# Kernel tuning notes

Measured on AMD Instinct MI355X. Metric: run time of the kernel, lower is better.

The kernel has to match this reference:

```python
import jax, jax.numpy as jnp
import numpy as np

EPS = 1e-5


def _in_relu(y):
    # instance norm (no affine, biased var, eps=1e-5) + ReLU, y: [B,C,H,W]
    mu = jnp.mean(y, axis=(-2, -1), keepdims=True)
    var = jnp.mean((y - mu) ** 2, axis=(-2, -1), keepdims=True)
    return jax.nn.relu((y - mu) * jax.lax.rsqrt(var + EPS))


def _conv3(x, w, b):
    # x: [C,H,W], w: [O,I,3,3] -> [O,H,W]
    y = jax.lax.conv_general_dilated(x[None], w, (1, 1), ((1, 1), (1, 1)),
                                     dimension_numbers=('NCHW', 'OIHW', 'NCHW'))[0]
    return y + b[:, None, None]


def _mod_block(x, W, b, mod):
    # per-sample weight modulation: mod[n] * W, then conv+IN+relu; x: [B,C,H,W], mod: [B,O,I,3,3]
    y = jax.vmap(lambda xi, mi: _conv3(xi, mi * W, b))(x, mod)
    return _in_relu(y)


def _maxpool2(x):
    return jax.lax.reduce_window(x, -jnp.inf, jax.lax.max, (1, 1, 2, 2), (1, 1, 2, 2), 'VALID')


def _up2(x):
    B, C, H, W = x.shape
    # bilinear, half-pixel centers == PyTorch align_corners=False
    return jax.image.resize(x, (B, C, 2 * H, 2 * W), method='bilinear')


def _conv1x1(x, w, b):
    y = jax.lax.conv_general_dilated(x, w, (1, 1), 'VALID',
                                     dimension_numbers=('NCHW', 'OIHW', 'NCHW'))
    return y + b[None, :, None, None]


def setup_inputs() -> dict:
    key = jax.random.key(0)
    B, H, W = 8, 256, 256
    ks = iter(jax.random.split(key, 64))
    d = {}
    d['us_query_input'] = jax.random.normal(next(ks), (B, 1, H, W), jnp.float32)
    d['ksp_query_imgs'] = jax.random.normal(next(ks), (B, H, W, 2), jnp.float32)
    d['ksp_mask_query'] = jax.random.uniform(next(ks), (B, H, W), jnp.float32)
    down_io = [(1, 32), (32, 64), (64, 128), (128, 256)]
    up_io = [(512, 128), (256, 64), (128, 32), (64, 32)]
    for i, (ci, co) in enumerate(down_io):
        d[f'down_mod_{i}'] = jax.random.normal(next(ks), (B, co, ci, 3, 3), jnp.float32)
        d[f'W_d{i}'] = 0.05 * jax.random.normal(next(ks), (co, ci, 3, 3), jnp.float32)
        d[f'b_d{i}'] = 0.05 * jax.random.normal(next(ks), (co,), jnp.float32)
    d['latent_mod'] = jax.random.normal(next(ks), (B, 256, 256, 3, 3), jnp.float32)
    d['W_lat'] = 0.05 * jax.random.normal(next(ks), (256, 256, 3, 3), jnp.float32)
    d['b_lat'] = 0.05 * jax.random.normal(next(ks), (256,), jnp.float32)
    for i, (ci, co) in enumerate(up_io):
        d[f'up_mod_{i}'] = jax.random.normal(next(ks), (B, co, ci, 3, 3), jnp.float32)
        d[f'W_u{i}'] = 0.05 * jax.random.normal(next(ks), (co, ci, 3, 3), jnp.float32)
        d[f'b_u{i}'] = 0.05 * jax.random.normal(next(ks), (co,), jnp.float32)
    d['w_c1'] = 0.05 * jax.random.normal(next(ks), (16, 32, 1, 1), jnp.float32)
    d['b_c1'] = 0.05 * jax.random.normal(next(ks), (16,), jnp.float32)
    d['w_c2'] = 0.05 * jax.random.normal(next(ks), (1, 16, 1, 1), jnp.float32)
    d['b_c2'] = 0.05 * jax.random.normal(next(ks), (1,), jnp.float32)
    d['w_c3'] = 0.05 * jax.random.normal(next(ks), (1, 1, 1, 1), jnp.float32)
    d['b_c3'] = 0.05 * jax.random.normal(next(ks), (1,), jnp.float32)
    return d


def reference(us_query_input, ksp_query_imgs, ksp_mask_query,
              down_mod_0, down_mod_1, down_mod_2, down_mod_3,
              latent_mod, up_mod_0, up_mod_1, up_mod_2, up_mod_3,
              W_d0, b_d0, W_d1, b_d1, W_d2, b_d2, W_d3, b_d3,
              W_lat, b_lat,
              W_u0, b_u0, W_u1, b_u1, W_u2, b_u2, W_u3, b_u3,
              w_c1, b_c1, w_c2, b_c2, w_c3, b_c3):
    x0 = us_query_input
    out = x0
    skips = []
    downs = [(W_d0, b_d0, down_mod_0), (W_d1, b_d1, down_mod_1),
             (W_d2, b_d2, down_mod_2), (W_d3, b_d3, down_mod_3)]
    for Wc, bc, m in downs:
        out = _mod_block(out, Wc, bc, m)
        skips.append(out)
        out = _maxpool2(out)
    out = _mod_block(out, W_lat, b_lat, latent_mod)
    ups = [(W_u0, b_u0, up_mod_0), (W_u1, b_u1, up_mod_1),
           (W_u2, b_u2, up_mod_2), (W_u3, b_u3, up_mod_3)]
    for Wc, bc, m in ups:
        out = _up2(out)
        out = jnp.concatenate([out, skips.pop()], axis=1)
        out = _mod_block(out, Wc, bc, m)
    out = _conv1x1(_conv1x1(_conv1x1(out, w_c1, b_c1), w_c2, b_c2), w_c3, b_c3)
    out = out + x0
    # FFT data consistency
    pred = out[:, 0]                                  # [B,H,W]
    kpred = jnp.fft.fft2(pred, norm='ortho')
    ksp = ksp_query_imgs[..., 0] + 1j * ksp_query_imgs[..., 1]
    upd = ksp_mask_query * ksp + (1.0 - ksp_mask_query) * kpred
    img = jnp.fft.ifft2(upd, norm='ortho')
    return jnp.real(img)[:, None].astype(jnp.float32)   # [B,1,H,W]
```

## Files before the change

### kernel.cpp

```cpp
#include <hip/hip_runtime.h>


#define EPS_IN 1e-5f

typedef __attribute__((ext_vector_type(8))) short short8;
typedef __attribute__((ext_vector_type(4))) short short4_t;
typedef __attribute__((ext_vector_type(4))) float f32x4;

__device__ __forceinline__ short f2bf(float f) {
    unsigned u = __float_as_uint(f);
    unsigned r = (u + 0x7fffu + ((u >> 16) & 1u)) >> 16;
    return (short)r;
}
__device__ __forceinline__ float bf2f(short s) {
    return __uint_as_float(((unsigned)(unsigned short)s) << 16);
}

__global__ void zero_f(float* __restrict__ p, int n)
{
    int i = blockIdx.x * 256 + threadIdx.x;
    if (i < n) p[i] = 0.f;
}

__global__ void make_wm(const float* __restrict__ W, const float* __restrict__ mod,
                        short* __restrict__ wm, int Co, int Ci)
{
    int idx = blockIdx.x * 256 + threadIdx.x;
    int total = 8 * Co * Ci;
    if (idx >= total) return;
    int ci = idx % Ci;
    int rem = idx / Ci;
    int co = rem % Co;
    int b = rem / Co;
    const float* wp = W + (size_t)(co * Ci + ci) * 9;
    const float* mp = mod + ((size_t)((size_t)b * Co + co) * Ci + ci) * 9;
#pragma unroll
    for (int k = 0; k < 9; ++k)
        wm[(((size_t)(b * 9 + k) * Co + co) * Ci + ci)] = f2bf(wp[k] * mp[k]);
}

template <int VR, int NCOG>
__global__ __launch_bounds__(256) void conv3x3_cl(
    const short* __restrict__ x1, int Ci1,
    const short* __restrict__ x2,
    const short* __restrict__ wm,
    short* __restrict__ y,
    float2* __restrict__ stats,
    int Ci, int Co, int H, int W)
{
    constexpr int TH = 4 * VR, SH = TH + 2, SW = 18;
    __shared__ short s_x[SH][SW][32];
    __shared__ float s_red[4][4][NCOG][4][2];

    const int tid = threadIdx.x;
    const int lane = tid & 63, wv = tid >> 6;
    const int m = lane & 15, g = lane >> 4;
    const int tilesx = W >> 4;
    const int tx0 = (blockIdx.x % tilesx) * 16;
    const int ty0 = (blockIdx.x / tilesx) * TH;
    const int co0 = blockIdx.y * (16 * NCOG);
    const int b = blockIdx.z;
    const int Ci2 = Ci - Ci1;

    f32x4 acc[NCOG][VR];
#pragma unroll
    for (int cg = 0; cg < NCOG; ++cg)
#pragma unroll
        for (int r = 0; r < VR; ++r) acc[cg][r] = (f32x4)0.f;

    const short* wmb = wm + (size_t)b * 9 * Co * Ci;

    for (int ci0 = 0; ci0 < Ci; ci0 += 32) {
        const short* src; int C, cb;
        if (ci0 < Ci1) { src = x1 + (size_t)b * H * W * Ci1; C = Ci1; cb = ci0; }
        else           { src = x2 + (size_t)b * H * W * Ci2; C = Ci2; cb = ci0 - Ci1; }
        __syncthreads();
        for (int idx = tid; idx < SH * SW * 4; idx += 256) {
            int gg = idx & 3, pos = idx >> 2;
            int yy = pos / SW, xx = pos - yy * SW;
            int gy = ty0 + yy - 1, gx = tx0 + xx - 1;
            short8 v = (short8)0;
            if (gy >= 0 && gy < H && gx >= 0 && gx < W)
                v = *(const short8*)(src + ((size_t)gy * W + gx) * C + cb + gg * 8);
            *(short8*)&s_x[yy][xx][(gg ^ (xx & 3)) * 8] = v;
        }
        __syncthreads();
#pragma unroll
        for (int t = 0; t < 9; ++t) {
            const int dy = t / 3, dx = t - 3 * (t / 3);
            const short* wr = wmb + ((size_t)t * Co + co0) * Ci + ci0 + g * 8;
            short8 a[NCOG];
#pragma unroll
            for (int cg = 0; cg < NCOG; ++cg)
                a[cg] = *(const short8*)(wr + (size_t)(cg * 16 + m) * Ci);
            const int xx = m + dx;
            const int sgo = (g ^ (xx & 3)) * 8;
#pragma unroll
            for (int r = 0; r < VR; ++r) {
                short8 bf = *(const short8*)&s_x[wv * VR + r + dy][xx][sgo];
#pragma unroll
                for (int cg = 0; cg < NCOG; ++cg)
                    acc[cg][r] = __builtin_amdgcn_mfma_f32_16x16x32_bf16(a[cg], bf, acc[cg][r], 0, 0, 0);
            }
        }
    }

    const int ox = tx0 + m;
#pragma unroll
    for (int cg = 0; cg < NCOG; ++cg)
#pragma unroll
        for (int r = 0; r < VR; ++r) {
            int oy = ty0 + wv * VR + r;
            short4_t o;
#pragma unroll
            for (int q = 0; q < 4; ++q) o[q] = f2bf(acc[cg][r][q]);
            *(short4_t*)(y + (((size_t)b * H + oy) * W + ox) * Co + co0 + cg * 16 + g * 4) = o;
        }

#pragma unroll
    for (int cg = 0; cg < NCOG; ++cg)
#pragma unroll
        for (int q = 0; q < 4; ++q) {
            float s = 0.f, s2 = 0.f;
#pragma unroll
            for (int r = 0; r < VR; ++r) { float v = acc[cg][r][q]; s += v; s2 += v * v; }
#pragma unroll
            for (int msk = 1; msk < 16; msk <<= 1) { s += __shfl_xor(s, msk); s2 += __shfl_xor(s2, msk); }
            if (m == 0) { s_red[wv][g][cg][q][0] = s; s_red[wv][g][cg][q][1] = s2; }
        }
    __syncthreads();
    for (int i = tid; i < 16 * NCOG; i += 256) {
        int q = i & 3, gg = (i >> 2) & 3, cg = i >> 4;
        float S = 0.f, S2 = 0.f;
#pragma unroll
        for (int w = 0; w < 4; ++w) { S += s_red[w][gg][cg][q][0]; S2 += s_red[w][gg][cg][q][1]; }
        float* sp = (float*)&stats[(size_t)b * Co + co0 + i];
        atomicAdd(sp, S); atomicAdd(sp + 1, S2);
    }
}

__global__ __launch_bounds__(256) void conv_d0_cl(
    const float* __restrict__ x0, const float* __restrict__ W,
    const float* __restrict__ mod, short* __restrict__ y,
    float2* __restrict__ stats)
{
    __shared__ float s[18][18];
    __shared__ float sw[32][9];
    __shared__ float s_red[4][32][2];
    const int tid = threadIdx.x;
    const int tx = tid & 15, ty = tid >> 4;
    const int tx0 = (blockIdx.x & 15) * 16, ty0 = (blockIdx.x >> 4) * 16;
    const int b = blockIdx.y;
    if (tid < 288) sw[tid / 9][tid % 9] = W[tid] * mod[b * 288 + tid];
    for (int pos = tid; pos < 18 * 18; pos += 256) {
        int yy = pos / 18, xx = pos - yy * 18;
        int gy = ty0 + yy - 1, gx = tx0 + xx - 1;
        bool inb = gy >= 0 && gy < 256 && gx >= 0 && gx < 256;
        s[yy][xx] = inb ? x0[((size_t)b << 16) + gy * 256 + gx] : 0.f;
    }
    __syncthreads();
    float v[3][3];
#pragma unroll
    for (int r = 0; r < 3; ++r)
#pragma unroll
        for (int c = 0; c < 3; ++c) v[r][c] = s[ty + r][tx + c];
    float vals[32];
#pragma unroll
    for (int co = 0; co < 32; ++co) {
        float a = 0.f;
#pragma unroll
        for (int r = 0; r < 3; ++r)
#pragma unroll
            for (int c = 0; c < 3; ++c) a = fmaf(v[r][c], sw[co][r * 3 + c], a);
        vals[co] = a;
    }
    short* yp = y + (((size_t)b * 256 + ty0 + ty) * 256 + tx0 + tx) * 32;
#pragma unroll
    for (int j = 0; j < 4; ++j) {
        short8 o;
#pragma unroll
        for (int e = 0; e < 8; ++e) o[e] = f2bf(vals[j * 8 + e]);
        *(short8*)(yp + j * 8) = o;
    }
    const int lane = tid & 63, wv = tid >> 6;
#pragma unroll
    for (int co = 0; co < 32; ++co) {
        float sm = vals[co], s2 = vals[co] * vals[co];
#pragma unroll
        for (int off = 32; off > 0; off >>= 1) { sm += __shfl_down(sm, off); s2 += __shfl_down(s2, off); }
        if (lane == 0) { s_red[wv][co][0] = sm; s_red[wv][co][1] = s2; }
    }
    __syncthreads();
    if (tid < 32) {
        float S = 0.f, S2 = 0.f;
#pragma unroll
        for (int w = 0; w < 4; ++w) { S += s_red[w][tid][0]; S2 += s_red[w][tid][1]; }
        float* sp = (float*)&stats[(size_t)b * 32 + tid];
        atomicAdd(sp, S); atomicAdd(sp + 1, S2);
    }
}

__global__ void maxpool_cl(short* __restrict__ in,
                           const float2* __restrict__ st, float invHW,
                           short* __restrict__ out,
                           int c8s, int ws, int hs, int total8)
{
    const int C = 8 << c8s;
    for (int idx = blockIdx.x * 256 + threadIdx.x; idx < total8; idx += gridDim.x * 256) {
        int c8 = idx & ((1 << c8s) - 1);
        int p = idx >> c8s;
        int x = p & ((1 << ws) - 1);
        int yy = (p >> ws) & ((1 << hs) - 1);
        int b = p >> (ws + hs);
        short* ip = in + (((size_t)b * (2 << hs) + 2 * yy) * (2 << ws) + 2 * x) * C + c8 * 8;
        size_t rs = (size_t)(2 << ws) * C;
        short8 v0 = *(const short8*)ip, v1 = *(const short8*)(ip + C);
        short8 v2 = *(const short8*)(ip + rs), v3 = *(const short8*)(ip + rs + C);
        short8 o, w0, w1, w2, w3;
#pragma unroll
        for (int e = 0; e < 8; ++e) {
            float2 sv = st[(size_t)b * C + c8 * 8 + e];
            float mu = sv.x * invHW;
            float rsig = rsqrtf(sv.y * invHW - mu * mu + EPS_IN);
            float n0 = fmaxf(0.f, (bf2f(v0[e]) - mu) * rsig);
            float n1 = fmaxf(0.f, (bf2f(v1[e]) - mu) * rsig);
            float n2 = fmaxf(0.f, (bf2f(v2[e]) - mu) * rsig);
            float n3 = fmaxf(0.f, (bf2f(v3[e]) - mu) * rsig);
            w0[e] = f2bf(n0); w1[e] = f2bf(n1); w2[e] = f2bf(n2); w3[e] = f2bf(n3);
            o[e] = f2bf(fmaxf(fmaxf(n0, n1), fmaxf(n2, n3)));
        }
        *(short8*)ip = w0;
        *(short8*)(ip + C) = w1;
        *(short8*)(ip + rs) = w2;
        *(short8*)(ip + rs + C) = w3;
        *(short8*)(out + (size_t)idx * 8) = o;
    }
}

__global__ void upsample_cl(const short* __restrict__ in,
                            const float2* __restrict__ st, float invHW,
                            short* __restrict__ out,
                            int c8s, int wsi, int hsi, int total8)
{
    const int C = 8 << c8s;
    const int Win = 1 << wsi, Hin = 1 << hsi;
    for (int idx = blockIdx.x * 256 + threadIdx.x; idx < total8; idx += gridDim.x * 256) {
        int c8 = idx & ((1 << c8s) - 1);
        int p = idx >> c8s;
        int x = p & (2 * Win - 1);
        int yy = (p >> (wsi + 1)) & (2 * Hin - 1);
        int b = p >> (wsi + 1 + hsi + 1);
        int xk = x >> 1, yk = yy >> 1;
        int xa, xb; float wxa;
        if (x & 1) { xa = xk; xb = (xk + 1 < Win) ? xk + 1 : Win - 1; wxa = 0.75f; }
        else       { xa = (xk > 0) ? xk - 1 : 0; xb = xk; wxa = 0.25f; }
        int ya, yb; float wya;
        if (yy & 1) { ya = yk; yb = (yk + 1 < Hin) ? yk + 1 : Hin - 1; wya = 0.75f; }
        else        { ya = (yk > 0) ? yk - 1 : 0; yb = yk; wya = 0.25f; }
        const short* ib = in + (size_t)b * Hin * Win * C + c8 * 8;
        short8 vaa = *(const short8*)(ib + ((size_t)ya * Win + xa) * C);
        short8 vab = *(const short8*)(ib + ((size_t)ya * Win + xb) * C);
        short8 vba = *(const short8*)(ib + ((size_t)yb * Win + xa) * C);
        short8 vbb = *(const short8*)(ib + ((size_t)yb * Win + xb) * C);
        short8 o;
#pragma unroll
        for (int e = 0; e < 8; ++e) {
            float2 sv = st[(size_t)b * C + c8 * 8 + e];
            float mu = sv.x * invHW;
            float rsig = rsqrtf(sv.y * invHW - mu * mu + EPS_IN);
            float aa = fmaxf(0.f, (bf2f(vaa[e]) - mu) * rsig);
            float ab = fmaxf(0.f, (bf2f(vab[e]) - mu) * rsig);
            float ba = fmaxf(0.f, (bf2f(vba[e]) - mu) * rsig);
            float bb = fmaxf(0.f, (bf2f(vbb[e]) - mu) * rsig);
            float r0 = wxa * aa + (1.f - wxa) * ab;
            float r1 = wxa * ba + (1.f - wxa) * bb;
            o[e] = f2bf(wya * r0 + (1.f - wya) * r1);
        }
        *(short8*)(out + (size_t)idx * 8) = o;
    }
}

__global__ void eff1x1(const float* __restrict__ w1, const float* __restrict__ b1,
                       const float* __restrict__ w2, const float* __restrict__ b2,
                       const float* __restrict__ w3, const float* __restrict__ b3,
                       float* __restrict__ eff)
{
    int t = threadIdx.x;
    if (t < 32) {
        float s = 0.f;
        for (int k = 0; k < 16; ++k) s += w2[k] * w1[k * 32 + t];
        eff[t] = w3[0] * s;
    }
    if (t == 32) {
        float s = 0.f;
        for (int k = 0; k < 16; ++k) s += w2[k] * b1[k];
        eff[32] = w3[0] * (s + b2[0]) + b3[0];
    }
}

__global__ __launch_bounds__(256) void final_pred_cl(
    const short* __restrict__ act, const float2* __restrict__ st, float invHW,
    const float* __restrict__ x0, const float* __restrict__ eff,
    float* __restrict__ pred)
{
    __shared__ float2 s_st[32];
    int idx = blockIdx.x * 256 + threadIdx.x;
    int b = idx >> 16;
    if (threadIdx.x < 32) {
        float2 v = st[(size_t)b * 32 + threadIdx.x];
        float mu = v.x * invHW;
        s_st[threadIdx.x] = make_float2(mu, rsqrtf(v.y * invHW - mu * mu + EPS_IN));
    }
    __syncthreads();
    const short8* a = (const short8*)(act + (size_t)idx * 32);
    float s = eff[32] + x0[idx];
#pragma unroll
    for (int j = 0; j < 4; ++j) {
        short8 v = a[j];
#pragma unroll
        for (int e = 0; e < 8; ++e) {
            float2 sv = s_st[j * 8 + e];
            float f = fmaxf(0.f, (bf2f(v[e]) - sv.x) * sv.y);
            s += eff[j * 8 + e] * f;
        }
    }
    pred[idx] = s;
}

__device__ __forceinline__ void fft256(float2* s, int tid, float sign)
{
    __syncthreads();
#pragma unroll
    for (int t = 0; t < 4; ++t) {
        int i = tid + t * 64;
        int r = __brev(i) >> 24;
        if (r > i) { float2 tmp = s[i]; s[i] = s[r]; s[r] = tmp; }
    }
    __syncthreads();
    for (int st = 1; st <= 8; ++st) {
        int m = 1 << st, half = m >> 1;
#pragma unroll
        for (int t = 0; t < 2; ++t) {
            int k = tid + t * 64;
            int g = k >> (st - 1), j = k & (half - 1);
            int i0 = (g << st) + j, i1 = i0 + half;
            float ang = sign * 6.283185307179586f * (float)j / (float)m;
            float sn, cs;
            __sincosf(ang, &sn, &cs);
            float2 a = s[i0], b = s[i1];
            float2 tt = make_float2(b.x * cs - b.y * sn, b.x * sn + b.y * cs);
            s[i0] = make_float2(a.x + tt.x, a.y + tt.y);
            s[i1] = make_float2(a.x - tt.x, a.y - tt.y);
        }
        __syncthreads();
    }
}

__global__ __launch_bounds__(64) void fft_rows_fwd(const float* __restrict__ pred,
                                                   float2* __restrict__ out)
{
    __shared__ float2 s[256];
    int row = blockIdx.x, tid = threadIdx.x;
    const float* p = pred + (size_t)row * 256;
    for (int i = tid; i < 256; i += 64) s[i] = make_float2(p[i], 0.f);
    fft256(s, tid, -1.f);
    float2* o = out + (size_t)row * 256;
    for (int i = tid; i < 256; i += 64) o[i] = s[i];
}

__global__ __launch_bounds__(64) void fft_cols_combine(float2* __restrict__ data,
                                                       const float* __restrict__ ksp,
                                                       const float* __restrict__ mask)
{
    __shared__ float2 s[256];
    int col = blockIdx.x & 255, b = blockIdx.x >> 8;
    int tid = threadIdx.x;
    float2* base = data + (size_t)b * 65536 + col;
    for (int i = tid; i < 256; i += 64) s[i] = base[(size_t)i * 256];
    fft256(s, tid, -1.f);
    for (int i = tid; i < 256; i += 64) {
        size_t mi = ((size_t)b * 256 + i) * 256 + col;
        float m = mask[mi];
        float2 kp = s[i];
        float kr = ksp[mi * 2], ki = ksp[mi * 2 + 1];
        s[i] = make_float2(m * kr + (1.f - m) * kp.x * (1.f / 256.f),
                           m * ki + (1.f - m) * kp.y * (1.f / 256.f));
    }
    fft256(s, tid, 1.f);
    for (int i = tid; i < 256; i += 64) base[(size_t)i * 256] = s[i];
}

__global__ __launch_bounds__(64) void fft_rows_inv(const float2* __restrict__ data,
                                                   float* __restrict__ out)
{
    __shared__ float2 s[256];
    int row = blockIdx.x, tid = threadIdx.x;
    const float2* p = data + (size_t)row * 256;
    for (int i = tid; i < 256; i += 64) s[i] = p[i];
    fft256(s, tid, 1.f);
    float* o = out + (size_t)row * 256;
    for (int i = tid; i < 256; i += 64) o[i] = s[i].x * (1.f / 256.f);
}

extern "C" void kernel_launch(void* const* d_in, const int* in_sizes, int n_in,
                              void* d_out, int out_size, void* d_ws, size_t ws_size,
                              hipStream_t stream)
{
    (void)in_sizes; (void)n_in; (void)out_size; (void)ws_size;

    const float* x0 = (const float*)d_in[0];
    const float* ksp = (const float*)d_in[1];
    const float* mask = (const float*)d_in[2];
    const float* mod_d[4] = {(const float*)d_in[3], (const float*)d_in[6],
                             (const float*)d_in[9], (const float*)d_in[12]};
    const float* W_d[4] = {(const float*)d_in[4], (const float*)d_in[7],
                           (const float*)d_in[10], (const float*)d_in[13]};
    const float* mod_lat = (const float*)d_in[15];
    const float* W_lat = (const float*)d_in[16];
    const float* mod_u[4] = {(const float*)d_in[18], (const float*)d_in[21],
                             (const float*)d_in[24], (const float*)d_in[27]};
    const float* W_u[4] = {(const float*)d_in[19], (const float*)d_in[22],
                           (const float*)d_in[25], (const float*)d_in[28]};
    const float* w_c1 = (const float*)d_in[30];
    const float* b_c1 = (const float*)d_in[31];
    const float* w_c2 = (const float*)d_in[32];
    const float* b_c2 = (const float*)d_in[33];
    const float* w_c3 = (const float*)d_in[34];
    const float* b_c3 = (const float*)d_in[35];

    short* sA  = (short*)d_ws;
    short* sB  = sA + 16777216;
    short* sk0 = sB + 16777216;
    short* sk1 = sk0 + 16777216;
    short* sk2 = sk1 + 8388608;
    short* sk3 = sk2 + 4194304;
    short* wm  = sk3 + 2097152;
    float* pred = (float*)(wm + 4718592);
    float2* cplx = (float2*)(pred + 524288);
    float2* stA = cplx + 524288;
    float* eff = (float*)(stA + 7936);

    float2* st_d0 = stA + 0;
    float2* st_d1 = stA + 256;
    float2* st_d2 = stA + 768;
    float2* st_d3 = stA + 1792;
    float2* st_lat = stA + 3840;
    float2* st_u0 = stA + 5888;
    float2* st_u1 = stA + 6912;
    float2* st_u2 = stA + 7424;
    float2* st_u3 = stA + 7680;

    const float i64k = 1.f / 65536.f, i16k = 1.f / 16384.f, i4k = 1.f / 4096.f,
                i1k = 1.f / 1024.f, i256 = 1.f / 256.f;

    dim3 blk(256);

    zero_f<<<62, blk, 0, stream>>>((float*)stA, 15872);
    eff1x1<<<1, 64, 0, stream>>>(w_c1, b_c1, w_c2, b_c2, w_c3, b_c3, eff);

    conv_d0_cl<<<dim3(256, 8), blk, 0, stream>>>(x0, W_d[0], mod_d[0], sk0, st_d0);
    maxpool_cl<<<2048, blk, 0, stream>>>(sk0, st_d0, i64k, sA, 2, 7, 7, 524288);

    make_wm<<<(8 * 64 * 32 + 255) / 256, blk, 0, stream>>>(W_d[1], mod_d[1], wm, 64, 32);
    conv3x3_cl<4, 4><<<dim3(64, 1, 8), blk, 0, stream>>>(sA, 32, sA, wm, sk1, st_d1, 32, 64, 128, 128);
    maxpool_cl<<<1024, blk, 0, stream>>>(sk1, st_d1, i16k, sA, 3, 6, 6, 262144);

    make_wm<<<(8 * 128 * 64 + 255) / 256, blk, 0, stream>>>(W_d[2], mod_d[2], wm, 128, 64);
    conv3x3_cl<2, 4><<<dim3(32, 2, 8), blk, 0, stream>>>(sA, 64, sA, wm, sk2, st_d2, 64, 128, 64, 64);
    maxpool_cl<<<512, blk, 0, stream>>>(sk2, st_d2, i4k, sA, 4, 5, 5, 131072);

    make_wm<<<(8 * 256 * 128 + 255) / 256, blk, 0, stream>>>(W_d[3], mod_d[3], wm, 256, 128);
    conv3x3_cl<2, 2><<<dim3(8, 8, 8), blk, 0, stream>>>(sA, 128, sA, wm, sk3, st_d3, 128, 256, 32, 32);
    maxpool_cl<<<256, blk, 0, stream>>>(sk3, st_d3, i1k, sA, 5, 4, 4, 65536);

    make_wm<<<(8 * 256 * 256 + 255) / 256, blk, 0, stream>>>(W_lat, mod_lat, wm, 256, 256);
    conv3x3_cl<2, 1><<<dim3(2, 16, 8), blk, 0, stream>>>(sA, 256, sA, wm, sB, st_lat, 256, 256, 16, 16);

    upsample_cl<<<1024, blk, 0, stream>>>(sB, st_lat, i256, sA, 5, 4, 4, 262144);
    make_wm<<<(8 * 128 * 512 + 255) / 256, blk, 0, stream>>>(W_u[0], mod_u[0], wm, 128, 512);
    conv3x3_cl<2, 1><<<dim3(8, 8, 8), blk, 0, stream>>>(sA, 256, sk3, wm, sB, st_u0, 512, 128, 32, 32);

    upsample_cl<<<2048, blk, 0, stream>>>(sB, st_u0, i1k, sA, 4, 5, 5, 524288);
    make_wm<<<(8 * 64 * 256 + 255) / 256, blk, 0, stream>>>(W_u[1], mod_u[1], wm, 64, 256);
    conv3x3_cl<2, 2><<<dim3(32, 2, 8), blk, 0, stream>>>(sA, 128, sk2, wm, sB, st_u1, 256, 64, 64, 64);

    upsample_cl<<<4096, blk, 0, stream>>>(sB, st_u1, i4k, sA, 3, 6, 6, 1048576);
    make_wm<<<(8 * 32 * 128 + 255) / 256, blk, 0, stream>>>(W_u[2], mod_u[2], wm, 32, 128);
    conv3x3_cl<4, 2><<<dim3(64, 1, 8), blk, 0, stream>>>(sA, 64, sk1, wm, sB, st_u2, 128, 32, 128, 128);

    upsample_cl<<<8192, blk, 0, stream>>>(sB, st_u2, i16k, sA, 2, 7, 7, 2097152);
    make_wm<<<(8 * 32 * 64 + 255) / 256, blk, 0, stream>>>(W_u[3], mod_u[3], wm, 32, 64);
    conv3x3_cl<4, 2><<<dim3(256, 1, 8), blk, 0, stream>>>(sA, 32, sk0, wm, sB, st_u3, 64, 32, 256, 256);

    final_pred_cl<<<2048, blk, 0, stream>>>(sB, st_u3, i64k, x0, eff, pred);

    fft_rows_fwd<<<2048, 64, 0, stream>>>(pred, cplx);
    fft_cols_combine<<<2048, 64, 0, stream>>>(cplx, ksp, mask);
    fft_rows_inv<<<2048, 64, 0, stream>>>(cplx, (float*)d_out);
}
```

Baseline: 518.3 us.

## Fuse upsample+IN into conv loads, batch weight modulation, fuse final pred into FFT

```diff
diff --git a/kernel.cpp b/kernel.cpp
--- a/kernel.cpp
+++ b/kernel.cpp
@@ -22,67 +22,136 @@
     if (i < n) p[i] = 0.f;
 }
 
-__global__ void make_wm(const float* __restrict__ W, const float* __restrict__ mod,
-                        short* __restrict__ wm, int Co, int Ci)
+struct WmJobs {
+    const float* W[8];
+    const float* mod[8];
+    short* wm[8];
+    int Co[8];
+    int Ci[8];
+    int cum[9];
+};
+
+__global__ void make_wm_all(WmJobs j)
 {
     int idx = blockIdx.x * 256 + threadIdx.x;
-    int total = 8 * Co * Ci;
-    if (idx >= total) return;
-    int ci = idx % Ci;
-    int rem = idx / Ci;
+    if (idx >= j.cum[8]) return;
+    int l = 0;
+    while (idx >= j.cum[l + 1]) ++l;
+    int local = idx - j.cum[l];
+    const int Ci = j.Ci[l], Co = j.Co[l];
+    int ci = local % Ci;
+    int rem = local / Ci;
     int co = rem % Co;
     int b = rem / Co;
-    const float* wp = W + (size_t)(co * Ci + ci) * 9;
-    const float* mp = mod + ((size_t)((size_t)b * Co + co) * Ci + ci) * 9;
+    const float* wp = j.W[l] + (size_t)(co * Ci + ci) * 9;
+    const float* mp = j.mod[l] + ((size_t)((size_t)b * Co + co) * Ci + ci) * 9;
+    short* wm = j.wm[l];
 #pragma unroll
     for (int k = 0; k < 9; ++k)
         wm[(((size_t)(b * 9 + k) * Co + co) * Ci + ci)] = f2bf(wp[k] * mp[k]);
 }
 
-template <int VR, int NCOG>
+template <int VR, int NCOG, bool UP>
 __global__ __launch_bounds__(256) void conv3x3_cl(
     const short* __restrict__ x1, int Ci1,
     const short* __restrict__ x2,
+    const float2* __restrict__ st1, float invHW1,
     const short* __restrict__ wm,
     short* __restrict__ y,
     float2* __restrict__ stats,
     int Ci, int Co, int H, int W)
 {
     constexpr int TH = 4 * VR, SH = TH + 2, SW = 18;
+    constexpr int STN = UP ? 256 : 1;
     __shared__ short s_x[SH][SW][32];
     __shared__ float s_red[4][4][NCOG][4][2];
+    __shared__ float2 s_st1[STN];
 
     const int tid = threadIdx.x;
     const int lane = tid & 63, wv = tid >> 6;
     const int m = lane & 15, g = lane >> 4;
+
+    const int b = blockIdx.x & 7;
+    int r = blockIdx.x >> 3;
+    const int nCoB = Co / (16 * NCOG);
+    const int coblk = r % nCoB;
+    const int tileId = r / nCoB;
     const int tilesx = W >> 4;
-    const int tx0 = (blockIdx.x % tilesx) * 16;
-    const int ty0 = (blockIdx.x / tilesx) * TH;
-    const int co0 = blockIdx.y * (16 * NCOG);
-    const int b = blockIdx.z;
+    const int tx0 = (tileId % tilesx) * 16;
+    const int ty0 = (tileId / tilesx) * TH;
+    const int co0 = coblk * (16 * NCOG);
     const int Ci2 = Ci - Ci1;
+    const int Hs = H >> 1, Ws = W >> 1;
+
+    if (UP) {
+        for (int i = tid; i < Ci1; i += 256) {
+            float2 v = st1[(size_t)b * Ci1 + i];
+            float mu = v.x * invHW1;
+            float var = v.y * invHW1 - mu * mu;
+            s_st1[i] = make_float2(mu, rsqrtf(var + EPS_IN));
+        }
+    }
 
     f32x4 acc[NCOG][VR];
 #pragma unroll
     for (int cg = 0; cg < NCOG; ++cg)
 #pragma unroll
-        for (int r = 0; r < VR; ++r) acc[cg][r] = (f32x4)0.f;
+        for (int rr = 0; rr < VR; ++rr) acc[cg][rr] = (f32x4)0.f;
 
     const short* wmb = wm + (size_t)b * 9 * Co * Ci;
+    const short* x1b = x1 + (size_t)b * (UP ? (size_t)Hs * Ws : (size_t)H * W) * Ci1;
+    const short* x2b = x2 + (size_t)b * H * W * Ci2;
 
     for (int ci0 = 0; ci0 < Ci; ci0 += 32) {
-        const short* src; int C, cb;
-        if (ci0 < Ci1) { src = x1 + (size_t)b * H * W * Ci1; C = Ci1; cb = ci0; }
-        else           { src = x2 + (size_t)b * H * W * Ci2; C = Ci2; cb = ci0 - Ci1; }
         __syncthreads();
-        for (int idx = tid; idx < SH * SW * 4; idx += 256) {
-            int gg = idx & 3, pos = idx >> 2;
-            int yy = pos / SW, xx = pos - yy * SW;
-            int gy = ty0 + yy - 1, gx = tx0 + xx - 1;
-            short8 v = (short8)0;
-            if (gy >= 0 && gy < H && gx >= 0 && gx < W)
-                v = *(const short8*)(src + ((size_t)gy * W + gx) * C + cb + gg * 8);
-            *(short8*)&s_x[yy][xx][(gg ^ (xx & 3)) * 8] = v;
+        if (UP && ci0 < Ci1) {
+            const int cb = ci0;
+            for (int idx = tid; idx < SH * SW * 4; idx += 256) {
+                int gg = idx & 3, pos = idx >> 2;
+                int yy = pos / SW, xx = pos - yy * SW;
+                int gy = ty0 + yy - 1, gx = tx0 + xx - 1;
+                short8 v = (short8)0;
+                if (gy >= 0 && gy < H && gx >= 0 && gx < W) {
+                    int xk = gx >> 1, yk = gy >> 1;
+                    int xo = gx & 1, yo = gy & 1;
+                    int xa = xo ? xk : (xk > 0 ? xk - 1 : 0);
+                    int xb = xo ? (xk + 1 < Ws ? xk + 1 : Ws - 1) : xk;
+                    float wxa = xo ? 0.75f : 0.25f;
+                    int ya = yo ? yk : (yk > 0 ? yk - 1 : 0);
+                    int yb = yo ? (yk + 1 < Hs ? yk + 1 : Hs - 1) : yk;
+                    float wya = yo ? 0.75f : 0.25f;
+                    const short* ib = x1b + cb + gg * 8;
+                    short8 vaa = *(const short8*)(ib + ((size_t)ya * Ws + xa) * Ci1);
+                    short8 vab = *(const short8*)(ib + ((size_t)ya * Ws + xb) * Ci1);
+                    short8 vba = *(const short8*)(ib + ((size_t)yb * Ws + xa) * Ci1);
+                    short8 vbb = *(const short8*)(ib + ((size_t)yb * Ws + xb) * Ci1);
+#pragma unroll
+                    for (int e = 0; e < 8; ++e) {
+                        float2 sv = s_st1[cb + gg * 8 + e];
+                        float aa = fmaxf(0.f, (bf2f(vaa[e]) - sv.x) * sv.y);
+                        float ab = fmaxf(0.f, (bf2f(vab[e]) - sv.x) * sv.y);
+                        float ba = fmaxf(0.f, (bf2f(vba[e]) - sv.x) * sv.y);
+                        float bb = fmaxf(0.f, (bf2f(vbb[e]) - sv.x) * sv.y);
+                        float r0 = wxa * aa + (1.f - wxa) * ab;
+                        float r1 = wxa * ba + (1.f - wxa) * bb;
+                        v[e] = f2bf(wya * r0 + (1.f - wya) * r1);
+                    }
+                }
+                *(short8*)&s_x[yy][xx][(gg ^ (xx & 3)) * 8] = v;
+            }
+        } else {
+            const short* src; int C, cb;
+            if (ci0 < Ci1) { src = x1b; C = Ci1; cb = ci0; }
+            else           { src = x2b; C = Ci2; cb = ci0 - Ci1; }
+            for (int idx = tid; idx < SH * SW * 4; idx += 256) {
+                int gg = idx & 3, pos = idx >> 2;
+                int yy = pos / SW, xx = pos - yy * SW;
+                int gy = ty0 + yy - 1, gx = tx0 + xx - 1;
+                short8 v = (short8)0;
+                if (gy >= 0 && gy < H && gx >= 0 && gx < W)
+                    v = *(const short8*)(src + ((size_t)gy * W + gx) * C + cb + gg * 8);
+                *(short8*)&s_x[yy][xx][(gg ^ (xx & 3)) * 8] = v;
+            }
         }
         __syncthreads();
 #pragma unroll
@@ -96,11 +165,11 @@
             const int xx = m + dx;
             const int sgo = (g ^ (xx & 3)) * 8;
 #pragma unroll
-            for (int r = 0; r < VR; ++r) {
-                short8 bf = *(const short8*)&s_x[wv * VR + r + dy][xx][sgo];
+            for (int rr = 0; rr < VR; ++rr) {
+                short8 bf = *(const short8*)&s_x[wv * VR + rr + dy][xx][sgo];
 #pragma unroll
                 for (int cg = 0; cg < NCOG; ++cg)
-                    acc[cg][r] = __builtin_amdgcn_mfma_f32_16x16x32_bf16(a[cg], bf, acc[cg][r], 0, 0, 0);
+                    acc[cg][rr] = __builtin_amdgcn_mfma_f32_16x16x32_bf16(a[cg], bf, acc[cg][rr], 0, 0, 0);
             }
         }
     }
@@ -109,11 +178,11 @@
 #pragma unroll
     for (int cg = 0; cg < NCOG; ++cg)
 #pragma unroll
-        for (int r = 0; r < VR; ++r) {
-            int oy = ty0 + wv * VR + r;
+        for (int rr = 0; rr < VR; ++rr) {
+            int oy = ty0 + wv * VR + rr;
             short4_t o;
 #pragma unroll
-            for (int q = 0; q < 4; ++q) o[q] = f2bf(acc[cg][r][q]);
+            for (int q = 0; q < 4; ++q) o[q] = f2bf(acc[cg][rr][q]);
             *(short4_t*)(y + (((size_t)b * H + oy) * W + ox) * Co + co0 + cg * 16 + g * 4) = o;
         }
 
@@ -123,7 +192,7 @@
         for (int q = 0; q < 4; ++q) {
             float s = 0.f, s2 = 0.f;
 #pragma unroll
-            for (int r = 0; r < VR; ++r) { float v = acc[cg][r][q]; s += v; s2 += v * v; }
+            for (int rr = 0; rr < VR; ++rr) { float v = acc[cg][rr][q]; s += v; s2 += v * v; }
 #pragma unroll
             for (int msk = 1; msk < 16; msk <<= 1) { s += __shfl_xor(s, msk); s2 += __shfl_xor(s2, msk); }
             if (m == 0) { s_red[wv][g][cg][q][0] = s; s_red[wv][g][cg][q][1] = s2; }
@@ -237,49 +306,6 @@
     }
 }
 
-__global__ void upsample_cl(const short* __restrict__ in,
-                            const float2* __restrict__ st, float invHW,
-                            short* __restrict__ out,
-                            int c8s, int wsi, int hsi, int total8)
-{
-    const int C = 8 << c8s;
-    const int Win = 1 << wsi, Hin = 1 << hsi;
-    for (int idx = blockIdx.x * 256 + threadIdx.x; idx < total8; idx += gridDim.x * 256) {
-        int c8 = idx & ((1 << c8s) - 1);
-        int p = idx >> c8s;
-        int x = p & (2 * Win - 1);
-        int yy = (p >> (wsi + 1)) & (2 * Hin - 1);
-        int b = p >> (wsi + 1 + hsi + 1);
-        int xk = x >> 1, yk = yy >> 1;
-        int xa, xb; float wxa;
-        if (x & 1) { xa = xk; xb = (xk + 1 < Win) ? xk + 1 : Win - 1; wxa = 0.75f; }
-        else       { xa = (xk > 0) ? xk - 1 : 0; xb = xk; wxa = 0.25f; }
-        int ya, yb; float wya;
-        if (yy & 1) { ya = yk; yb = (yk + 1 < Hin) ? yk + 1 : Hin - 1; wya = 0.75f; }
-        else        { ya = (yk > 0) ? yk - 1 : 0; yb = yk; wya = 0.25f; }
-        const short* ib = in + (size_t)b * Hin * Win * C + c8 * 8;
-        short8 vaa = *(const short8*)(ib + ((size_t)ya * Win + xa) * C);
-        short8 vab = *(const short8*)(ib + ((size_t)ya * Win + xb) * C);
-        short8 vba = *(const short8*)(ib + ((size_t)yb * Win + xa) * C);
-        short8 vbb = *(const short8*)(ib + ((size_t)yb * Win + xb) * C);
-        short8 o;
-#pragma unroll
-        for (int e = 0; e < 8; ++e) {
-            float2 sv = st[(size_t)b * C + c8 * 8 + e];
-            float mu = sv.x * invHW;
-            float rsig = rsqrtf(sv.y * invHW - mu * mu + EPS_IN);
-            float aa = fmaxf(0.f, (bf2f(vaa[e]) - mu) * rsig);
-            float ab = fmaxf(0.f, (bf2f(vab[e]) - mu) * rsig);
-            float ba = fmaxf(0.f, (bf2f(vba[e]) - mu) * rsig);
-            float bb = fmaxf(0.f, (bf2f(vbb[e]) - mu) * rsig);
-            float r0 = wxa * aa + (1.f - wxa) * ab;
-            float r1 = wxa * ba + (1.f - wxa) * bb;
-            o[e] = f2bf(wya * r0 + (1.f - wya) * r1);
-        }
-        *(short8*)(out + (size_t)idx * 8) = o;
-    }
-}
-
 __global__ void eff1x1(const float* __restrict__ w1, const float* __restrict__ b1,
                        const float* __restrict__ w2, const float* __restrict__ b2,
                        const float* __restrict__ w3, const float* __restrict__ b3,
@@ -296,35 +322,6 @@
         for (int k = 0; k < 16; ++k) s += w2[k] * b1[k];
         eff[32] = w3[0] * (s + b2[0]) + b3[0];
     }
-}
-
-__global__ __launch_bounds__(256) void final_pred_cl(
-    const short* __restrict__ act, const float2* __restrict__ st, float invHW,
-    const float* __restrict__ x0, const float* __restrict__ eff,
-    float* __restrict__ pred)
-{
-    __shared__ float2 s_st[32];
-    int idx = blockIdx.x * 256 + threadIdx.x;
-    int b = idx >> 16;
-    if (threadIdx.x < 32) {
-        float2 v = st[(size_t)b * 32 + threadIdx.x];
-        float mu = v.x * invHW;
-        s_st[threadIdx.x] = make_float2(mu, rsqrtf(v.y * invHW - mu * mu + EPS_IN));
-    }
-    __syncthreads();
-    const short8* a = (const short8*)(act + (size_t)idx * 32);
-    float s = eff[32] + x0[idx];
-#pragma unroll
-    for (int j = 0; j < 4; ++j) {
-        short8 v = a[j];
-#pragma unroll
-        for (int e = 0; e < 8; ++e) {
-            float2 sv = s_st[j * 8 + e];
-            float f = fmaxf(0.f, (bf2f(v[e]) - sv.x) * sv.y);
-            s += eff[j * 8 + e] * f;
-        }
-    }
-    pred[idx] = s;
 }
 
 __device__ __forceinline__ void fft256(float2* s, int tid, float sign)
@@ -356,15 +353,41 @@
     }
 }
 
-__global__ __launch_bounds__(64) void fft_rows_fwd(const float* __restrict__ pred,
-                                                   float2* __restrict__ out)
+__global__ __launch_bounds__(64) void final_fft_rows(
+    const short* __restrict__ act, const float2* __restrict__ st, float invHW,
+    const float* __restrict__ x0, const float* __restrict__ eff,
+    float2* __restrict__ cplx)
 {
     __shared__ float2 s[256];
-    int row = blockIdx.x, tid = threadIdx.x;
-    const float* p = pred + (size_t)row * 256;
-    for (int i = tid; i < 256; i += 64) s[i] = make_float2(p[i], 0.f);
+    __shared__ float2 sst[32];
+    __shared__ float seff[33];
+    const int row = blockIdx.x, tid = threadIdx.x;
+    const int b = row >> 8, yy = row & 255;
+    if (tid < 32) {
+        float2 v = st[(size_t)b * 32 + tid];
+        float mu = v.x * invHW;
+        sst[tid] = make_float2(mu, rsqrtf(v.y * invHW - mu * mu + EPS_IN));
+    }
+    if (tid < 33) seff[tid] = eff[tid];
+    __syncthreads();
+#pragma unroll
+    for (int k = 0; k < 4; ++k) {
+        int x = k * 64 + tid;
+        const short8* a = (const short8*)(act + (((size_t)b * 256 + yy) * 256 + x) * 32);
+        float sacc = seff[32] + x0[((size_t)b << 16) + (yy << 8) + x];
+#pragma unroll
+        for (int j = 0; j < 4; ++j) {
+            short8 v = a[j];
+#pragma unroll
+            for (int e = 0; e < 8; ++e) {
+                float2 sv = sst[j * 8 + e];
+                sacc += seff[j * 8 + e] * fmaxf(0.f, (bf2f(v[e]) - sv.x) * sv.y);
+            }
+        }
+        s[x] = make_float2(sacc, 0.f);
+    }
     fft256(s, tid, -1.f);
-    float2* o = out + (size_t)row * 256;
+    float2* o = cplx + (size_t)row * 256;
     for (int i = tid; i < 256; i += 64) o[i] = s[i];
 }
 
@@ -434,9 +457,15 @@
     short* sk1 = sk0 + 16777216;
     short* sk2 = sk1 + 8388608;
     short* sk3 = sk2 + 4194304;
-    short* wm  = sk3 + 2097152;
-    float* pred = (float*)(wm + 4718592);
-    float2* cplx = (float2*)(pred + 524288);
+    short* wm_d1 = sk3 + 2097152;
+    short* wm_d2 = wm_d1 + 147456;
+    short* wm_d3 = wm_d2 + 589824;
+    short* wm_lat = wm_d3 + 2359296;
+    short* wm_u0 = wm_lat + 4718592;
+    short* wm_u1 = wm_u0 + 4718592;
+    short* wm_u2 = wm_u1 + 1179648;
+    short* wm_u3 = wm_u2 + 294912;
+    float2* cplx = (float2*)(wm_u3 + 147456);
     float2* stA = cplx + 524288;
     float* eff = (float*)(stA + 7936);
 
@@ -458,43 +487,41 @@
     zero_f<<<62, blk, 0, stream>>>((float*)stA, 15872);
     eff1x1<<<1, 64, 0, stream>>>(w_c1, b_c1, w_c2, b_c2, w_c3, b_c3, eff);
 
+    WmJobs jobs;
+    const float* Wl[8]  = {W_d[1], W_d[2], W_d[3], W_lat, W_u[0], W_u[1], W_u[2], W_u[3]};
+    const float* Ml[8]  = {mod_d[1], mod_d[2], mod_d[3], mod_lat, mod_u[0], mod_u[1], mod_u[2], mod_u[3]};
+    short* WMl[8] = {wm_d1, wm_d2, wm_d3, wm_lat, wm_u0, wm_u1, wm_u2, wm_u3};
+    int Col[8] = {64, 128, 256, 256, 128, 64, 32, 32};
+    int Cil[8] = {32, 64, 128, 256, 512, 256, 128, 64};
+    jobs.cum[0] = 0;
+    for (int l = 0; l < 8; ++l) {
+        jobs.W[l] = Wl[l]; jobs.mod[l] = Ml[l]; jobs.wm[l] = WMl[l];
+        jobs.Co[l] = Col[l]; jobs.Ci[l] = Cil[l];
+        jobs.cum[l + 1] = jobs.cum[l] + 8 * Col[l] * Cil[l];
+    }
+    make_wm_all<<<(jobs.cum[8] + 255) / 256, blk, 0, stream>>>(jobs);
+
     conv_d0_cl<<<dim3(256, 8), blk, 0, stream>>>(x0, W_d[0], mod_d[0], sk0, st_d0);
     maxpool_cl<<<2048, blk, 0, stream>>>(sk0, st_d0, i64k, sA, 2, 7, 7, 524288);
 
-    make_wm<<<(8 * 64 * 32 + 255) / 256, blk, 0, stream>>>(W_d[1], mod_d[1], wm, 64, 32);
-    conv3x3_cl<4, 4><<<dim3(64, 1, 8), blk, 0, stream>>>(sA, 32, sA, wm, sk1, st_d1, 32, 64, 128, 128);
+    conv3x3_cl<4, 4, false><<<512, blk, 0, stream>>>(sA, 32, sA, stA, 0.f, wm_d1, sk1, st_d1, 32, 64, 128, 128);
     maxpool_cl<<<1024, blk, 0, stream>>>(sk1, st_d1, i16k, sA, 3, 6, 6, 262144);
 
-    make_wm<<<(8 * 128 * 64 + 255) / 256, blk, 0, stream>>>(W_d[2], mod_d[2], wm, 128, 64);
-    conv3x3_cl<2, 4><<<dim3(32, 2, 8), blk, 0, stream>>>(sA, 64, sA, wm, sk2, st_d2, 64, 128, 64, 64);
+    conv3x3_cl<2, 4, false><<<512, blk, 0, stream>>>(sA, 64, sA, stA, 0.f, wm_d2, sk2, st_d2, 64, 128, 64, 64);
     maxpool_cl<<<512, blk, 0, stream>>>(sk2, st_d2, i4k, sA, 4, 5, 5, 131072);
 
-    make_wm<<<(8 * 256 * 128 + 255) / 256, blk, 0, stream>>>(W_d[3], mod_d[3], wm, 256, 128);
-    conv3x3_cl<2, 2><<<dim3(8, 8, 8), blk, 0, stream>>>(sA, 128, sA, wm, sk3, st_d3, 128, 256, 32, 32);
+    conv3x3_cl<2, 2, false><<<512, blk, 0, stream>>>(sA, 128, sA, stA, 0.f, wm_d3, sk3, st_d3, 128, 256, 32, 32);
     maxpool_cl<<<256, blk, 0, stream>>>(sk3, st_d3, i1k, sA, 5, 4, 4, 65536);
 
-    make_wm<<<(8 * 256 * 256 + 255) / 256, blk, 0, stream>>>(W_lat, mod_lat, wm, 256, 256);
-    conv3x3_cl<2, 1><<<dim3(2, 16, 8), blk, 0, stream>>>(sA, 256, sA, wm, sB, st_lat, 256, 256, 16, 16);
-
-    upsample_cl<<<1024, blk, 0, stream>>>(sB, st_lat, i256, sA, 5, 4, 4, 262144);
-    make_wm<<<(8 * 128 * 512 + 255) / 256, blk, 0, stream>>>(W_u[0], mod_u[0], wm, 128, 512);
-    conv3x3_cl<2, 1><<<dim3(8, 8, 8), blk, 0, stream>>>(sA, 256, sk3, wm, sB, st_u0, 512, 128, 32, 32);
-
-    upsample_cl<<<2048, blk, 0, stream>>>(sB, st_u0, i1k, sA, 4, 5, 5, 524288);
-    make_wm<<<(8 * 64 * 256 + 255) / 256, blk, 0, stream>>>(W_u[1], mod_u[1], wm, 64, 256);
-    conv3x3_cl<2, 2><<<dim3(32, 2, 8), blk, 0, stream>>>(sA, 128, sk2, wm, sB, st_u1, 256, 64, 64, 64);
-
-    upsample_cl<<<4096, blk, 0, stream>>>(sB, st_u1, i4k, sA, 3, 6, 6, 1048576);
-    make_wm<<<(8 * 32 * 128 + 255) / 256, blk, 0, stream>>>(W_u[2], mod_u[2], wm, 32, 128);
-    conv3x3_cl<4, 2><<<dim3(64, 1, 8), blk, 0, stream>>>(sA, 64, sk1, wm, sB, st_u2, 128, 32, 128, 128);
-
-    upsample_cl<<<8192, blk, 0, stream>>>(sB, st_u2, i16k, sA, 2, 7, 7, 2097152);
-    make_wm<<<(8 * 32 * 64 + 255) / 256, blk, 0, stream>>>(W_u[3], mod_u[3], wm, 32, 64);
-    conv3x3_cl<4, 2><<<dim3(256, 1, 8), blk, 0, stream>>>(sA, 32, sk0, wm, sB, st_u3, 64, 32, 256, 256);
-
-    final_pred_cl<<<2048, blk, 0, stream>>>(sB, st_u3, i64k, x0, eff, pred);
-
-    fft_rows_fwd<<<2048, 64, 0, stream>>>(pred, cplx);
+    conv3x3_cl<2, 1, false><<<256, blk, 0, stream>>>(sA, 256, sA, stA, 0.f, wm_lat, sB, st_lat, 256, 256, 16, 16);
+
+    conv3x3_cl<2, 1, true><<<512, blk, 0, stream>>>(sB, 256, sk3, st_lat, i256, wm_u0, sA, st_u0, 512, 128, 32, 32);
+    conv3x3_cl<2, 2, true><<<512, blk, 0, stream>>>(sA, 128, sk2, st_u0, i1k, wm_u1, sB, st_u1, 256, 64, 64, 64);
+    conv3x3_cl<4, 2, true><<<512, blk, 0, stream>>>(sB, 64, sk1, st_u1, i4k, wm_u2, sA, st_u2, 128, 32, 128, 128);
+    conv3x3_cl<4, 2, true><<<2048, blk, 0, stream>>>(sA, 32, sk0, st_u2, i16k, wm_u3, sB, st_u3, 64, 32, 256, 256);
+
+    final_fft_rows<<<2048, 64, 0, stream>>>(sB, st_u3, i64k, x0, eff, cplx);
+
     fft_cols_combine<<<2048, 64, 0, stream>>>(cplx, ksp, mask);
     fft_rows_inv<<<2048, 64, 0, stream>>>(cplx, (float*)d_out);
 }
```

Measured after the change: 501.8 us. 3.2% less time.
